# Kernel tuning notes

Hardware: AMD Instinct MI355X
Metric: run time of the kernel (lower is better)

The kernel has to match this reference:

```python
import jax, jax.numpy as jnp
import numpy as np
from jax import lax

B, T, DEC, ENC, ATTN, K = 32, 4096, 1024, 1024, 512, 10


def setup_inputs() -> dict:
    key = jax.random.key(0)
    ks = jax.random.split(key, 10)
    s = 0.02
    return {
        "query": jax.random.normal(ks[0], (B, 1, DEC), dtype=jnp.float32),
        "value": jax.random.normal(ks[1], (B, T, ENC), dtype=jnp.float32),
        "last_align": jax.random.uniform(ks[2], (B, T), dtype=jnp.float32),
        "conv_w": jax.random.normal(ks[3], (K, 1, 3), dtype=jnp.float32) * s,
        "conv_b": jnp.zeros((K,), dtype=jnp.float32),
        "WQ": jax.random.normal(ks[4], (ATTN, DEC), dtype=jnp.float32) * s,
        "WV": jax.random.normal(ks[5], (ATTN, ENC), dtype=jnp.float32) * s,
        "WU": jax.random.normal(ks[6], (ATTN, K), dtype=jnp.float32) * s,
        "bias": jax.random.uniform(ks[7], (ATTN,), minval=-0.1, maxval=0.1, dtype=jnp.float32),
        "fc_w": jax.random.normal(ks[8], (1, ATTN), dtype=jnp.float32) * s,
    }


def reference(query, value, last_align, conv_w, conv_b, WQ, WV, WU, bias, fc_w):
    # Conv1d(1 -> k, ks=3, pad=1): [B,1,T] -> [B,k,T] -> [B,T,k]
    conv_feat = lax.conv_general_dilated(
        last_align[:, None, :], conv_w, window_strides=(1,), padding=[(1, 1)]
    ) + conv_b[None, :, None]
    conv_feat = jnp.transpose(conv_feat, (0, 2, 1))  # [B,T,K]

    q = jnp.einsum('bqd,ad->bqa', query, WQ)      # [B,1,ATTN]
    v = jnp.einsum('bte,ae->bta', value, WV)      # [B,T,ATTN]
    u = jnp.einsum('btk,ak->bta', conv_feat, WU)  # [B,T,ATTN]

    attn_score = jnp.einsum('bta,oa->bto', jnp.tanh(q + v + u + bias), fc_w)[..., 0]  # [B,T]

    # smoothing=True path: sigmoid then normalize to sum 1
    attn_score = jax.nn.sigmoid(attn_score)
    align = attn_score / jnp.sum(attn_score, axis=-1, keepdims=True)  # [B,T]

    context = jnp.einsum('bt,bte->be', align, value)  # [B,ENC]
    return context, align
```

## Files before the change

kernel.cpp:

```cpp
#include <hip/hip_runtime.h>
#include <hip/hip_bf16.h>


typedef __attribute__((ext_vector_type(8))) short bf8_t;
typedef __attribute__((ext_vector_type(4))) float f4_t;

__device__ inline unsigned short f2bf(float f) {
    union { float f; unsigned u; } v; v.f = f;
    unsigned u = v.u + 0x7fffu + ((v.u >> 16) & 1u);
    return (unsigned short)(u >> 16);
}

__global__ void k_wv2bf(const float* __restrict__ wv, unsigned short* __restrict__ out) {
    int i = blockIdx.x * 256 + threadIdx.x;
    float4 v = ((const float4*)wv)[i];
    uint2 p;
    p.x = (unsigned)f2bf(v.x) | ((unsigned)f2bf(v.y) << 16);
    p.y = (unsigned)f2bf(v.z) | ((unsigned)f2bf(v.w) << 16);
    ((uint2*)out)[i] = p;
}

__global__ void k_qb2(const float* __restrict__ query, const float* __restrict__ WQ,
                      const float* __restrict__ bias, const float* __restrict__ convb,
                      const float* __restrict__ WU, float* __restrict__ qb2) {
    __shared__ float qs[1024];
    int b = blockIdx.x;
    for (int d = threadIdx.x; d < 1024; d += 256) qs[d] = query[b * 1024 + d];
    __syncthreads();
    for (int a = threadIdx.x; a < 512; a += 256) {
        float s = bias[a];
        for (int k = 0; k < 10; k++) s += convb[k] * WU[a * 10 + k];
        const float4* wq = (const float4*)(WQ + a * 1024);
        const float4* q4 = (const float4*)qs;
        float acc = 0.f;
        for (int d = 0; d < 256; d++) {
            float4 w = wq[d]; float4 q = q4[d];
            acc += w.x * q.x + w.y * q.y + w.z * q.z + w.w * q.w;
        }
        qb2[b * 512 + a] = s + acc;
    }
}

__global__ void k_a012(const float* __restrict__ cw, const float* __restrict__ WU,
                       float* __restrict__ a012) {
    int a = blockIdx.x * 256 + threadIdx.x;
    if (a < 512) {
        float s0 = 0.f, s1 = 0.f, s2 = 0.f;
        for (int k = 0; k < 10; k++) {
            float w = WU[a * 10 + k];
            s0 += cw[k * 3 + 0] * w;
            s1 += cw[k * 3 + 1] * w;
            s2 += cw[k * 3 + 2] * w;
        }
        a012[a] = s0; a012[512 + a] = s1; a012[1024 + a] = s2;
    }
}

__global__ __launch_bounds__(512, 2) void k_gemm(
    const float* __restrict__ value, const unsigned short* __restrict__ wvbf,
    const float* __restrict__ qb2, const float* __restrict__ a012,
    const float* __restrict__ fcw, const float* __restrict__ la,
    float* __restrict__ sigbuf, float* __restrict__ bsum) {
    __shared__ unsigned short As[128][48];
    __shared__ unsigned short Bs[512][48];
    __shared__ float rowLa[3][128];
    __shared__ float scoreRed[128][4];

    const int tid = threadIdx.x;
    const int lane = tid & 63;
    const int wave = tid >> 6;
    const int wm = (wave & 1) * 64;
    const int wn = (wave >> 1) * 128;
    const int rowBase = blockIdx.x * 128;
    const int bIdx = blockIdx.x >> 5;

    f4_t acc[4][8];
#pragma unroll
    for (int i = 0; i < 4; i++)
#pragma unroll
        for (int j = 0; j < 8; j++) acc[i][j] = (f4_t)0.0f;

    const int ar = tid >> 2;
    const int ac = (tid & 3) * 8;
    const float4* aptr = (const float4*)(value + (size_t)(rowBase + ar) * 1024 + ac);
    const int br = tid >> 2;
    const int bc = (tid & 3) * 8;

    const int koff = (lane >> 4) * 8;
    const int am = wm + (lane & 15);

    for (int kk = 0; kk < 32; ++kk) {
        const int k0 = kk * 32;
        float4 av0 = aptr[(k0 >> 2)];
        float4 av1 = aptr[(k0 >> 2) + 1];
        uint4 bv[4];
#pragma unroll
        for (int p = 0; p < 4; p++)
            bv[p] = *(const uint4*)(wvbf + (size_t)(p * 128 + br) * 1024 + k0 + bc);

        __syncthreads();
        uint4 ap;
        ap.x = (unsigned)f2bf(av0.x) | ((unsigned)f2bf(av0.y) << 16);
        ap.y = (unsigned)f2bf(av0.z) | ((unsigned)f2bf(av0.w) << 16);
        ap.z = (unsigned)f2bf(av1.x) | ((unsigned)f2bf(av1.y) << 16);
        ap.w = (unsigned)f2bf(av1.z) | ((unsigned)f2bf(av1.w) << 16);
        *(uint4*)&As[ar][ac] = ap;
#pragma unroll
        for (int p = 0; p < 4; p++) *(uint4*)&Bs[p * 128 + br][bc] = bv[p];
        __syncthreads();

        bf8_t af[4];
#pragma unroll
        for (int i = 0; i < 4; i++) af[i] = *(const bf8_t*)&As[am + i * 16][koff];
#pragma unroll
        for (int j = 0; j < 8; j++) {
            bf8_t bfv = *(const bf8_t*)&Bs[wn + j * 16 + (lane & 15)][koff];
#pragma unroll
            for (int i = 0; i < 4; i++)
                acc[i][j] = __builtin_amdgcn_mfma_f32_16x16x32_bf16(af[i], bfv, acc[i][j], 0, 0, 0);
        }
    }

    if (tid < 128) {
        int grow = rowBase + tid;
        int t = grow & 4095;
        rowLa[0][tid] = (t == 0) ? 0.f : la[grow - 1];
        rowLa[1][tid] = la[grow];
        rowLa[2][tid] = (t == 4095) ? 0.f : la[grow + 1];
    }
    float qv[8], c0[8], c1[8], c2[8], fv[8];
#pragma unroll
    for (int j = 0; j < 8; j++) {
        int a = wn + j * 16 + (lane & 15);
        qv[j] = qb2[bIdx * 512 + a];
        c0[j] = a012[a]; c1[j] = a012[512 + a]; c2[j] = a012[1024 + a];
        fv[j] = fcw[a];
    }
    __syncthreads();

    const int q4 = lane >> 4;
#pragma unroll
    for (int i = 0; i < 4; i++) {
#pragma unroll
        for (int r = 0; r < 4; r++) {
            int row = wm + i * 16 + q4 * 4 + r;
            float lm = rowLa[0][row], l0 = rowLa[1][row], lp = rowLa[2][row];
            float s = 0.f;
#pragma unroll
            for (int j = 0; j < 8; j++) {
                float x = acc[i][j][r] + qv[j] + lm * c0[j] + l0 * c1[j] + lp * c2[j];
                float e = __expf(2.f * x);
                s += fv[j] * (1.f - 2.f / (e + 1.f));
            }
            s += __shfl_xor(s, 1); s += __shfl_xor(s, 2);
            s += __shfl_xor(s, 4); s += __shfl_xor(s, 8);
            if ((lane & 15) == 0) scoreRed[row][wave >> 1] = s;
        }
    }
    __syncthreads();

    if (tid < 128) {
        float full = scoreRed[tid][0] + scoreRed[tid][1] + scoreRed[tid][2] + scoreRed[tid][3];
        float sg = 1.f / (1.f + __expf(-full));
        sigbuf[rowBase + tid] = sg;
        float w = sg;
        w += __shfl_xor(w, 1); w += __shfl_xor(w, 2); w += __shfl_xor(w, 4);
        w += __shfl_xor(w, 8); w += __shfl_xor(w, 16); w += __shfl_xor(w, 32);
        if (lane == 0) atomicAdd(&bsum[bIdx], w);
    }
}

__global__ void k_align(const float* __restrict__ sig, const float* __restrict__ bsum,
                        float* __restrict__ out) {
    int i = blockIdx.x * 256 + threadIdx.x;
    out[i] = sig[i] / bsum[i >> 12];
}

__global__ __launch_bounds__(256) void k_ctx(const float* __restrict__ value,
                                             const float* __restrict__ alignw,
                                             float* __restrict__ ctx) {
    int e = blockIdx.x * 256 + threadIdx.x;
    int b = blockIdx.z;
    int t0 = blockIdx.y * 512;
    const float* vp = value + (size_t)(b * 4096 + t0) * 1024 + e;
    const float* wp = alignw + b * 4096 + t0;
    float a0 = 0.f, a1 = 0.f, a2 = 0.f, a3 = 0.f;
    for (int t = 0; t < 512; t += 4) {
        a0 += wp[t + 0] * vp[(size_t)(t + 0) * 1024];
        a1 += wp[t + 1] * vp[(size_t)(t + 1) * 1024];
        a2 += wp[t + 2] * vp[(size_t)(t + 2) * 1024];
        a3 += wp[t + 3] * vp[(size_t)(t + 3) * 1024];
    }
    atomicAdd(&ctx[b * 1024 + e], a0 + a1 + a2 + a3);
}

extern "C" void kernel_launch(void* const* d_in, const int* in_sizes, int n_in,
                              void* d_out, int out_size, void* d_ws, size_t ws_size,
                              hipStream_t stream) {
    const float* query = (const float*)d_in[0];
    const float* value = (const float*)d_in[1];
    const float* la    = (const float*)d_in[2];
    const float* convw = (const float*)d_in[3];
    const float* convb = (const float*)d_in[4];
    const float* WQ    = (const float*)d_in[5];
    const float* WV    = (const float*)d_in[6];
    const float* WU    = (const float*)d_in[7];
    const float* bias  = (const float*)d_in[8];
    const float* fcw   = (const float*)d_in[9];
    float* out = (float*)d_out;

    char* ws = (char*)d_ws;
    float* sigbuf = (float*)ws;
    float* qb2    = (float*)(ws + 524288);
    float* a012   = (float*)(ws + 589824);
    float* bsum   = (float*)(ws + 595968);
    unsigned short* wvbf = (unsigned short*)(ws + 596096);

    hipMemsetAsync(bsum, 0, 32 * sizeof(float), stream);
    hipMemsetAsync(out, 0, 32 * 1024 * sizeof(float), stream);

    k_wv2bf<<<512, 256, 0, stream>>>(WV, wvbf);
    k_qb2<<<32, 256, 0, stream>>>(query, WQ, bias, convb, WU, qb2);
    k_a012<<<2, 256, 0, stream>>>(convw, WU, a012);
    k_gemm<<<1024, 512, 0, stream>>>(value, wvbf, qb2, a012, fcw, la, sigbuf, bsum);
    k_align<<<512, 256, 0, stream>>>(sigbuf, bsum, out + 32768);
    k_ctx<<<dim3(4, 8, 32), 256, 0, stream>>>(value, out + 32768, out);
}
```

Measured before the change: 1.260 ms.

## Double-buffer WV tiles via global_load_lds with swizzled LDS and vectorize context reduction

The bf16 WV copy is pre-tiled into 64-wide K tiles with an XOR swizzle. The GEMM now streams those tiles straight into double-buffered LDS with global_load_lds while it computes on the current tile. The value tile is prefetched into registers one step ahead and converted to bf16 into a swizzled A buffer, and K steps are 64 wide with manual waitcnt and barriers. The context kernel is reworked to use float4 loads over 128-token chunks. The much larger LDS footprint (about 145KB) limits the GEMM to one block per CU, and the hand-placed waitcnts are fragile.

```diff
diff --git a/kernel.cpp b/kernel.cpp
--- a/kernel.cpp
+++ b/kernel.cpp
@@ -1,5 +1,4 @@
 #include <hip/hip_runtime.h>
-#include <hip/hip_bf16.h>
 
 
 typedef __attribute__((ext_vector_type(8))) short bf8_t;
@@ -10,14 +9,28 @@
     unsigned u = v.u + 0x7fffu + ((v.u >> 16) & 1u);
     return (unsigned short)(u >> 16);
 }
+__device__ inline unsigned pk2(float x, float y) {
+    return (unsigned)f2bf(x) | ((unsigned)f2bf(y) << 16);
+}
+
+__device__ inline void gload16(const void* g, void* l) {
+    __builtin_amdgcn_global_load_lds(
+        (const __attribute__((address_space(1))) unsigned int*)g,
+        (__attribute__((address_space(3))) unsigned int*)l, 16, 0, 0);
+}
 
 __global__ void k_wv2bf(const float* __restrict__ wv, unsigned short* __restrict__ out) {
     int i = blockIdx.x * 256 + threadIdx.x;
-    float4 v = ((const float4*)wv)[i];
-    uint2 p;
-    p.x = (unsigned)f2bf(v.x) | ((unsigned)f2bf(v.y) << 16);
-    p.y = (unsigned)f2bf(v.z) | ((unsigned)f2bf(v.w) << 16);
-    ((uint2*)out)[i] = p;
+    int a = i >> 7;
+    int e0 = (i & 127) << 3;
+    const float4* src = (const float4*)(wv + (size_t)a * 1024 + e0);
+    float4 v0 = src[0], v1 = src[1];
+    uint4 p;
+    p.x = pk2(v0.x, v0.y); p.y = pk2(v0.z, v0.w);
+    p.z = pk2(v1.x, v1.y); p.w = pk2(v1.z, v1.w);
+    int kt = e0 >> 6;
+    int kx = (e0 & 63) ^ ((a & 7) << 3);
+    *(uint4*)(out + (size_t)kt * 32768 + a * 64 + kx) = p;
 }
 
 __global__ void k_qb2(const float* __restrict__ query, const float* __restrict__ WQ,
@@ -61,8 +74,8 @@
     const float* __restrict__ qb2, const float* __restrict__ a012,
     const float* __restrict__ fcw, const float* __restrict__ la,
     float* __restrict__ sigbuf, float* __restrict__ bsum) {
-    __shared__ unsigned short As[128][48];
-    __shared__ unsigned short Bs[512][48];
+    __shared__ unsigned short Bs[2][512 * 64];
+    __shared__ unsigned short As[128 * 64];
     __shared__ float rowLa[3][128];
     __shared__ float scoreRed[128][4];
 
@@ -80,45 +93,91 @@
 #pragma unroll
         for (int j = 0; j < 8; j++) acc[i][j] = (f4_t)0.0f;
 
-    const int ar = tid >> 2;
-    const int ac = (tid & 3) * 8;
-    const float4* aptr = (const float4*)(value + (size_t)(rowBase + ar) * 1024 + ac);
-    const int br = tid >> 2;
-    const int bc = (tid & 3) * 8;
-
-    const int koff = (lane >> 4) * 8;
+    const int ar = tid >> 3;
+    const int ak = (tid & 7) * 8;
+    const float* aSrc0 = value + (size_t)(rowBase + ar) * 1024 + ak;
+    const float* aSrc1 = aSrc0 + (size_t)64 * 1024;
+    const int aswz = ak ^ ((ar & 7) << 3);
+    const int aOff0 = ar * 64 + aswz;
+    const int aOff1 = (ar + 64) * 64 + aswz;
+
+    const int sw = (lane & 7) << 3;
+    const int ko = (lane >> 4) * 8;
     const int am = wm + (lane & 15);
-
-    for (int kk = 0; kk < 32; ++kk) {
-        const int k0 = kk * 32;
-        float4 av0 = aptr[(k0 >> 2)];
-        float4 av1 = aptr[(k0 >> 2) + 1];
-        uint4 bv[4];
-#pragma unroll
-        for (int p = 0; p < 4; p++)
-            bv[p] = *(const uint4*)(wvbf + (size_t)(p * 128 + br) * 1024 + k0 + bc);
-
-        __syncthreads();
-        uint4 ap;
-        ap.x = (unsigned)f2bf(av0.x) | ((unsigned)f2bf(av0.y) << 16);
-        ap.y = (unsigned)f2bf(av0.z) | ((unsigned)f2bf(av0.w) << 16);
-        ap.z = (unsigned)f2bf(av1.x) | ((unsigned)f2bf(av1.y) << 16);
-        ap.w = (unsigned)f2bf(av1.z) | ((unsigned)f2bf(av1.w) << 16);
-        *(uint4*)&As[ar][ac] = ap;
-#pragma unroll
-        for (int p = 0; p < 4; p++) *(uint4*)&Bs[p * 128 + br][bc] = bv[p];
-        __syncthreads();
-
-        bf8_t af[4];
-#pragma unroll
-        for (int i = 0; i < 4; i++) af[i] = *(const bf8_t*)&As[am + i * 16][koff];
-#pragma unroll
-        for (int j = 0; j < 8; j++) {
-            bf8_t bfv = *(const bf8_t*)&Bs[wn + j * 16 + (lane & 15)][koff];
+    const int bn = wn + (lane & 15);
+
+    float4 a0, a1, a2, a3;
+
+    a0 = *(const float4*)(aSrc0);
+    a1 = *(const float4*)(aSrc0 + 4);
+    a2 = *(const float4*)(aSrc1);
+    a3 = *(const float4*)(aSrc1 + 4);
+    {
+        const unsigned short* gB = wvbf;
+        unsigned short* lB = &Bs[0][0];
+#pragma unroll
+        for (int c = 0; c < 8; c++)
+            gload16(gB + (c * 512 + tid) * 8, lB + (c * 512 + tid) * 8);
+    }
+    asm volatile("s_waitcnt vmcnt(8)" ::: "memory");
+    {
+        uint4 p0, p1;
+        p0.x = pk2(a0.x, a0.y); p0.y = pk2(a0.z, a0.w);
+        p0.z = pk2(a1.x, a1.y); p0.w = pk2(a1.z, a1.w);
+        p1.x = pk2(a2.x, a2.y); p1.y = pk2(a2.z, a2.w);
+        p1.z = pk2(a3.x, a3.y); p1.w = pk2(a3.z, a3.w);
+        *(uint4*)&As[aOff0] = p0;
+        *(uint4*)&As[aOff1] = p1;
+    }
+    asm volatile("s_waitcnt vmcnt(0) lgkmcnt(0)" ::: "memory");
+    __builtin_amdgcn_s_barrier();
+    __builtin_amdgcn_sched_barrier(0);
+
+    for (int kt = 0; kt < 16; ++kt) {
+        const int cur = kt & 1;
+        if (kt < 15) {
+            const float* s0 = aSrc0 + (kt + 1) * 64;
+            const float* s1 = aSrc1 + (kt + 1) * 64;
+            a0 = *(const float4*)(s0);
+            a1 = *(const float4*)(s0 + 4);
+            a2 = *(const float4*)(s1);
+            a3 = *(const float4*)(s1 + 4);
+            const unsigned short* gB = wvbf + (size_t)(kt + 1) * 32768;
+            unsigned short* lB = &Bs[cur ^ 1][0];
+#pragma unroll
+            for (int c = 0; c < 8; c++)
+                gload16(gB + (c * 512 + tid) * 8, lB + (c * 512 + tid) * 8);
+        }
+        const unsigned short* Bp = &Bs[cur][0];
+#pragma unroll
+        for (int ks = 0; ks < 2; ++ks) {
+            const int kq = (ks * 32 + ko) ^ sw;
+            bf8_t af[4];
 #pragma unroll
             for (int i = 0; i < 4; i++)
-                acc[i][j] = __builtin_amdgcn_mfma_f32_16x16x32_bf16(af[i], bfv, acc[i][j], 0, 0, 0);
-        }
+                af[i] = *(const bf8_t*)&As[(am + i * 16) * 64 + kq];
+#pragma unroll
+            for (int j = 0; j < 8; j++) {
+                bf8_t bv = *(const bf8_t*)&Bp[(bn + j * 16) * 64 + kq];
+#pragma unroll
+                for (int i = 0; i < 4; i++)
+                    acc[i][j] = __builtin_amdgcn_mfma_f32_16x16x32_bf16(af[i], bv, acc[i][j], 0, 0, 0);
+            }
+        }
+        __builtin_amdgcn_s_barrier();
+        if (kt < 15) {
+            asm volatile("s_waitcnt vmcnt(8)" ::: "memory");
+            uint4 p0, p1;
+            p0.x = pk2(a0.x, a0.y); p0.y = pk2(a0.z, a0.w);
+            p0.z = pk2(a1.x, a1.y); p0.w = pk2(a1.z, a1.w);
+            p1.x = pk2(a2.x, a2.y); p1.y = pk2(a2.z, a2.w);
+            p1.z = pk2(a3.x, a3.y); p1.w = pk2(a3.z, a3.w);
+            *(uint4*)&As[aOff0] = p0;
+            *(uint4*)&As[aOff1] = p1;
+            asm volatile("s_waitcnt vmcnt(0) lgkmcnt(0)" ::: "memory");
+        }
+        __builtin_amdgcn_s_barrier();
+        __builtin_amdgcn_sched_barrier(0);
     }
 
     if (tid < 128) {
@@ -179,19 +238,22 @@
 __global__ __launch_bounds__(256) void k_ctx(const float* __restrict__ value,
                                              const float* __restrict__ alignw,
                                              float* __restrict__ ctx) {
-    int e = blockIdx.x * 256 + threadIdx.x;
-    int b = blockIdx.z;
-    int t0 = blockIdx.y * 512;
-    const float* vp = value + (size_t)(b * 4096 + t0) * 1024 + e;
+    int b = blockIdx.y;
+    int t0 = blockIdx.x * 128;
+    const float* vp = value + (size_t)(b * 4096 + t0) * 1024 + threadIdx.x * 4;
     const float* wp = alignw + b * 4096 + t0;
-    float a0 = 0.f, a1 = 0.f, a2 = 0.f, a3 = 0.f;
-    for (int t = 0; t < 512; t += 4) {
-        a0 += wp[t + 0] * vp[(size_t)(t + 0) * 1024];
-        a1 += wp[t + 1] * vp[(size_t)(t + 1) * 1024];
-        a2 += wp[t + 2] * vp[(size_t)(t + 2) * 1024];
-        a3 += wp[t + 3] * vp[(size_t)(t + 3) * 1024];
-    }
-    atomicAdd(&ctx[b * 1024 + e], a0 + a1 + a2 + a3);
+    float4 acc; acc.x = acc.y = acc.z = acc.w = 0.f;
+#pragma unroll 4
+    for (int t = 0; t < 128; ++t) {
+        float w = wp[t];
+        float4 v = *(const float4*)(vp + (size_t)t * 1024);
+        acc.x += w * v.x; acc.y += w * v.y; acc.z += w * v.z; acc.w += w * v.w;
+    }
+    float* cp = ctx + b * 1024 + threadIdx.x * 4;
+    atomicAdd(cp + 0, acc.x);
+    atomicAdd(cp + 1, acc.y);
+    atomicAdd(cp + 2, acc.z);
+    atomicAdd(cp + 3, acc.w);
 }
 
 extern "C" void kernel_launch(void* const* d_in, const int* in_sizes, int n_in,
@@ -219,10 +281,10 @@
     hipMemsetAsync(bsum, 0, 32 * sizeof(float), stream);
     hipMemsetAsync(out, 0, 32 * 1024 * sizeof(float), stream);
 
-    k_wv2bf<<<512, 256, 0, stream>>>(WV, wvbf);
+    k_wv2bf<<<256, 256, 0, stream>>>(WV, wvbf);
     k_qb2<<<32, 256, 0, stream>>>(query, WQ, bias, convb, WU, qb2);
     k_a012<<<2, 256, 0, stream>>>(convw, WU, a012);
     k_gemm<<<1024, 512, 0, stream>>>(value, wvbf, qb2, a012, fcw, la, sigbuf, bsum);
     k_align<<<512, 256, 0, stream>>>(sigbuf, bsum, out + 32768);
-    k_ctx<<<dim3(4, 8, 32), 256, 0, stream>>>(value, out + 32768, out);
-}
+    k_ctx<<<dim3(32, 32), 256, 0, stream>>>(value, out + 32768, out);
+}
```

Measured after the change: 1.018 ms. 1.24x faster.
